# Performance work log

Hardware: AMD Instinct MI355X
Metric: run time of the kernel (lower is better)

The kernel has to match this reference:

```python
import jax, jax.numpy as jnp
import numpy as np
from jax import lax

B, V, M, C, CM, D = 48, 16, 32, 48, 8, 128
VOCAB_V, VOCAB_M, OUT = 2000, 1000, 256


def setup_inputs() -> dict:
    key = jax.random.key(0)
    ks = jax.random.split(key, 22)
    s = 0.1  # keep GRU gates out of saturation
    return {
        "visit_ids": jax.random.randint(ks[0], (3, B, V, C), 0, VOCAB_V),
        "mon_ids": jax.random.randint(ks[1], (4, B, V, M, CM), 0, VOCAB_M),
        "weight_vals": jax.random.uniform(ks[2], (B, V)),
        "age_vals": jax.random.uniform(ks[3], (B, V)),
        "emb_visit": jax.random.normal(ks[4], (3, VOCAB_V, D)) * s,
        "emb_mon": jax.random.normal(ks[5], (4, VOCAB_M, D)) * s,
        "mgru_Wih": jax.random.normal(ks[6], (5, 3 * D, D)) * s,
        "mgru_Whh": jax.random.normal(ks[7], (5, 3 * D, D)) * s,
        "mgru_bih": jax.random.normal(ks[8], (5, 3 * D)) * s,
        "mgru_bhh": jax.random.normal(ks[9], (5, 3 * D)) * s,
        "vgru_Wih": jax.random.normal(ks[10], (7, 3 * D, D)) * s,
        "vgru_Whh": jax.random.normal(ks[11], (7, 3 * D, D)) * s,
        "vgru_bih": jax.random.normal(ks[12], (7, 3 * D)) * s,
        "vgru_bhh": jax.random.normal(ks[13], (7, 3 * D)) * s,
        "fc_weight_w": jax.random.normal(ks[14], (D, 1)) * s,
        "fc_weight_b": jax.random.normal(ks[15], (D,)) * s,
        "fc_age_w": jax.random.normal(ks[16], (D, 1)) * s,
        "fc_age_b": jax.random.normal(ks[17], (D,)) * s,
        "fc_out_w": jax.random.normal(ks[18], (OUT, 7 * D)) * s,
        "fc_out_b": jax.random.normal(ks[19], (OUT,)) * s,
    }


def gru_last(x, Wih, Whh, bih, bhh):
    """torch.nn.GRU(batch_first=True), return final hidden [N, D]."""
    xi = jnp.einsum('ntd,ed->nte', x, Wih) + bih  # [N, T, 3D] input projections
    h0 = jnp.zeros((x.shape[0], Whh.shape[1]), x.dtype)

    def step(h, gi):
        gh = h @ Whh.T + bhh
        ir, iz, inn = jnp.split(gi, 3, axis=-1)
        hr, hz, hn = jnp.split(gh, 3, axis=-1)
        r = jax.nn.sigmoid(ir + hr)
        z = jax.nn.sigmoid(iz + hz)
        n = jnp.tanh(inn + r * hn)
        return (1.0 - z) * n + z * h, None

    hT, _ = lax.scan(step, h0, jnp.swapaxes(xi, 0, 1))
    return hT


def reference(visit_ids, mon_ids, weight_vals, age_vals, emb_visit, emb_mon,
              mgru_Wih, mgru_Whh, mgru_bih, mgru_bhh,
              vgru_Wih, vgru_Whh, vgru_bih, vgru_bhh,
              fc_weight_w, fc_weight_b, fc_age_w, fc_age_b,
              fc_out_w, fc_out_b):
    # padding_idx=0 -> zero embedding row (dropout in eval mode = identity)
    ev = emb_visit.at[:, 0].set(0.0)
    em = emb_mon.at[:, 0].set(0.0)

    # visit-event embedding-bag: sum over code dim -> [B, V, D] per feature
    visit_origin = [jnp.sum(ev[k][visit_ids[k]], axis=2) for k in range(3)]

    def run_stream(t, mi, vi):
        # monitor-level GRU over M, then visit-level GRU over V
        h1 = gru_last(t, mgru_Wih[mi], mgru_Whh[mi], mgru_bih[mi], mgru_bhh[mi])
        h2 = gru_last(h1.reshape(B, V, D),
                      vgru_Wih[vi], vgru_Whh[vi], vgru_bih[vi], vgru_bhh[vi])
        return h2  # [B, D]

    # output slots in dict-insertion order: lab_item, cond, proc, drug, inj_item, weight, age
    slots = [None] * 7
    for p in range(2):  # (lab_item, lab_value), (inj_item, inj_value)
        # elementwise item*value embedding, summed over codes -> [B*V, M, D]
        mon = jnp.sum(em[2 * p][mon_ids[2 * p]] * em[2 * p + 1][mon_ids[2 * p + 1]],
                      axis=3).reshape(B * V, M, D)
        slots[0 if p == 0 else 4] = run_stream(mon, p, p)
        for k in range(3):  # visit features repeated along monitor dim
            t = jnp.broadcast_to(visit_origin[k][:, :, None, :],
                                 (B, V, M, D)).reshape(B * V, M, D)
            h = run_stream(t, 2 + k, 2 + k)
            slots[1 + k] = h if slots[1 + k] is None else slots[1 + k] + h

    # weight / age: Linear(1->D), zero-mask, visit-level GRU
    for vals, w, b, vi, slot in ((weight_vals, fc_weight_w, fc_weight_b, 5, 5),
                                 (age_vals, fc_age_w, fc_age_b, 6, 6)):
        xf = vals.reshape(-1, 1)
        h = (xf @ w.T + b) * (xf != 0)
        slots[slot] = gru_last(h.reshape(B, V, D),
                               vgru_Wih[vi], vgru_Whh[vi], vgru_bih[vi], vgru_bhh[vi])

    patient_emb = jnp.concatenate(slots, axis=-1)  # [B, 7D]
    return jax.nn.relu(patient_emb) @ fc_out_w.T + fc_out_b
```

## Files before the change

### kernel.cpp

```cpp
#include <hip/hip_runtime.h>
#include <stdint.h>


typedef unsigned short u16;
typedef uint32_t u32;
typedef short bf8 __attribute__((ext_vector_type(8)));
typedef float f4 __attribute__((ext_vector_type(4)));

static __device__ __forceinline__ float bf2f(u16 b){ u32 u=((u32)b)<<16; float f; __builtin_memcpy(&f,&u,4); return f; }
static __device__ __forceinline__ u16 f2bf(float f){ u32 u; __builtin_memcpy(&u,&f,4); u32 r=(u+0x7fffu+((u>>16)&1u))>>16; return (u16)r; }
static __device__ __forceinline__ float bflo(u32 u){ u32 x=u<<16; float f; __builtin_memcpy(&f,&x,4); return f; }
static __device__ __forceinline__ float bfhi(u32 u){ u32 x=u&0xffff0000u; float f; __builtin_memcpy(&f,&x,4); return f; }
static __device__ __forceinline__ f4 mfma16(bf8 a, bf8 b, f4 c){ return __builtin_amdgcn_mfma_f32_16x16x32_bf16(a,b,c,0,0,0); }
static __device__ __forceinline__ float sigm(float x){ return 1.0f/(1.0f+__expf(-x)); }
static __device__ __forceinline__ float tanh_f(float x){ return 1.0f-2.0f/(__expf(2.0f*x)+1.0f); }

__global__ __launch_bounds__(256) void k_prep(const float* __restrict__ s0, const float* __restrict__ s1,
                                              const float* __restrict__ s2, const float* __restrict__ s3,
                                              const float* __restrict__ s4,
                                              u16* __restrict__ d0, u16* __restrict__ d1,
                                              u16* __restrict__ d2, u16* __restrict__ d3,
                                              u16* __restrict__ d4){
  int y = blockIdx.y;
  const float* src = y==0?s0 : y==1?s1 : y==2?s2 : y==3?s3 : s4;
  u16* dst         = y==0?d0 : y==1?d1 : y==2?d2 : y==3?d3 : d4;
  int n4 = (y<2 ? 245760 : y<4 ? 344064 : 512000) >> 2;
  int i = blockIdx.x*256 + threadIdx.x;
  if (i < n4){
    float4 v = *(const float4*)(src + (size_t)i*4);
    ushort4 o = { f2bf(v.x), f2bf(v.y), f2bf(v.z), f2bf(v.w) };
    *(ushort4*)(dst + (size_t)i*4) = o;
  }
}

__global__ __launch_bounds__(128) void k_front(const int* __restrict__ vids,
                                               const float* __restrict__ embv,
                                               const float* __restrict__ wv, const float* __restrict__ av,
                                               const float* __restrict__ ww, const float* __restrict__ wb,
                                               const float* __restrict__ aw, const float* __restrict__ ab,
                                               u16* __restrict__ vis_org, u16* __restrict__ hin2T){
  __shared__ int ids[48];
  int y = blockIdx.y, row = blockIdx.x, d = threadIdx.x;
  if (y < 3){
    if (d < 48) ids[d] = vids[((size_t)y*768 + row)*48 + d];
    __syncthreads();
    const float* eb = embv + (size_t)y*2000*128;
    float acc = 0.f;
    #pragma unroll 4
    for (int c = 0; c < 48; ++c){ int id = ids[c]; if (id) acc += eb[(size_t)id*128 + d]; }
    vis_org[((size_t)y*768 + row)*128 + d] = f2bf(acc);
  } else {
    int sidx = y - 3;
    const float* vals = sidx ? av : wv;
    const float* wgt  = sidx ? aw : ww;
    const float* bias = sidx ? ab : wb;
    float v = vals[row];
    float h = (v != 0.f) ? (v * wgt[d] + bias[d]) : 0.f;
    int b = row >> 4, vv = row & 15;
    hin2T[((size_t)(5+sidx)*768 + (size_t)vv*48 + b)*128 + d] = f2bf(h);
  }
}

__global__ __launch_bounds__(256) void k_embed_mon(const int* __restrict__ mids,
                                                   const u16* __restrict__ embm_b,
                                                   u16* __restrict__ mon_xT){
  int p = blockIdx.y;
  int rid = threadIdx.x >> 5, lane32 = threadIdx.x & 31, d0 = lane32*4;
  __shared__ int ids[8][16];
  if (threadIdx.x < 128){
    int rr = threadIdx.x >> 4, c = threadIdx.x & 15;
    int f = 2*p + (c>>3), cm = c & 7;
    ids[rr][c] = mids[((size_t)f*24576 + (size_t)blockIdx.x*8 + rr)*8 + cm];
  }
  __syncthreads();
  const u16* e1 = embm_b + (size_t)(2*p)*1000*128;
  const u16* e2 = embm_b + (size_t)(2*p+1)*1000*128;
  float a0=0.f,a1=0.f,a2=0.f,a3=0.f;
  #pragma unroll
  for (int c = 0; c < 8; ++c){
    int i1 = ids[rid][c], i2 = ids[rid][8+c];
    if (i1 && i2){
      uint2 a = *(const uint2*)(e1 + (size_t)i1*128 + d0);
      uint2 b = *(const uint2*)(e2 + (size_t)i2*128 + d0);
      a0 += bflo(a.x)*bflo(b.x); a1 += bfhi(a.x)*bfhi(b.x);
      a2 += bflo(a.y)*bflo(b.y); a3 += bfhi(a.y)*bfhi(b.y);
    }
  }
  size_t nm = (size_t)blockIdx.x*8 + rid;
  int bv = (int)(nm >> 5), m = (int)(nm & 31);
  ushort4 o = { f2bf(a0), f2bf(a1), f2bf(a2), f2bf(a3) };
  *(ushort4*)(mon_xT + (size_t)p*24576*128 + ((size_t)m*768 + bv)*128 + d0) = o;
}

#define ALOAD(D, tt) { const u16* p_ = ap + (size_t)(tt)*rstride; \
  D[0]=*(const bf8*)(p_); D[1]=*(const bf8*)(p_+32); D[2]=*(const bf8*)(p_+64); D[3]=*(const bf8*)(p_+96); }

#define STEP(D, tt, FIRST) { \
  f4 g0={biv[0],biv[0],biv[0],biv[0]}; \
  f4 g1={biv[1],biv[1],biv[1],biv[1]}; \
  f4 g2={biv[2],biv[2],biv[2],biv[2]}; \
  g0=mfma16(D[0],wfi[0][0],g0); g0=mfma16(D[1],wfi[0][1],g0); \
  g0=mfma16(D[2],wfi[0][2],g0); g0=mfma16(D[3],wfi[0][3],g0); \
  g1=mfma16(D[0],wfi[1][0],g1); g1=mfma16(D[1],wfi[1][1],g1); \
  g1=mfma16(D[2],wfi[1][2],g1); g1=mfma16(D[3],wfi[1][3],g1); \
  g2=mfma16(D[0],wfi[2][0],g2); g2=mfma16(D[1],wfi[2][1],g2); \
  g2=mfma16(D[2],wfi[2][2],g2); g2=mfma16(D[3],wfi[2][3],g2); \
  { int tl_ = ((tt)+2 < T) ? (tt)+2 : 0; ALOAD(D, tl_); } \
  f4 a0={bhv[0],bhv[0],bhv[0],bhv[0]}; \
  f4 a1={bhv[1],bhv[1],bhv[1],bhv[1]}; \
  f4 a2={bhv[2],bhv[2],bhv[2],bhv[2]}; \
  if (!(FIRST)){ \
    bf8 hf0 = *(const bf8*)&hlds[cur][lr][0*32+lq*8]; \
    bf8 hf1 = *(const bf8*)&hlds[cur][lr][1*32+lq*8]; \
    bf8 hf2 = *(const bf8*)&hlds[cur][lr][2*32+lq*8]; \
    bf8 hf3 = *(const bf8*)&hlds[cur][lr][3*32+lq*8]; \
    a0=mfma16(hf0,wfh[0][0],a0); a0=mfma16(hf1,wfh[0][1],a0); \
    a0=mfma16(hf2,wfh[0][2],a0); a0=mfma16(hf3,wfh[0][3],a0); \
    a1=mfma16(hf0,wfh[1][0],a1); a1=mfma16(hf1,wfh[1][1],a1); \
    a1=mfma16(hf2,wfh[1][2],a1); a1=mfma16(hf3,wfh[1][3],a1); \
    a2=mfma16(hf0,wfh[2][0],a2); a2=mfma16(hf1,wfh[2][1],a2); \
    a2=mfma16(hf2,wfh[2][2],a2); a2=mfma16(hf3,wfh[2][3],a2); \
  } \
  int nxt_ = cur ^ 1; \
  _Pragma("unroll") \
  for (int r = 0; r < 4; ++r){ \
    float rr2 = sigm(g0[r] + a0[r]); \
    float zz  = sigm(g1[r] + a1[r]); \
    float nn  = tanh_f(g2[r] + rr2*a2[r]); \
    float hv  = (1.0f - zz)*nn + zz*hp[r]; hp[r] = hv; \
    hlds[nxt_][lq*4+r][w*16+lr] = f2bf(hv); \
  } \
  __syncthreads(); cur = nxt_; }

__global__ __launch_bounds__(512, 1) void k_gru(int mode,
    const u16* __restrict__ Asrc, const u16* __restrict__ Asrc2,
    const u16* __restrict__ Wih, const float* __restrict__ bih,
    const u16* __restrict__ Whh, const float* __restrict__ bhh,
    u16* __restrict__ hout, int T){
  int s = blockIdx.y, g = blockIdx.x;
  const u16* A; size_t rstride; u16* ho; int widx;
  if (mode == 0){
    if (s < 2){ A = Asrc + (size_t)s*24576*128; rstride = 768*128; }
    else      { A = Asrc2 + (size_t)(s-2)*768*128; rstride = 0; }
    widx = s;
    int slot = (0x32140u >> (4*s)) & 15;
    ho = hout + (size_t)slot*768*128;
  } else {
    A = Asrc + (size_t)s*768*128; rstride = 48*128;
    widx = (0x6514320u >> (4*s)) & 15;
    ho = hout + (size_t)s*48*128;
  }
  const u16* Wi = Wih + (size_t)widx*384*128;
  const u16* Wh = Whh + (size_t)widx*384*128;
  const float* bi = bih + (size_t)widx*384;
  const float* bh = bhh + (size_t)widx*384;

  int w = threadIdx.x >> 6, l = threadIdx.x & 63;
  int lr = l & 15, lq = l >> 4;

  bf8 wfi[3][4], wfh[3][4]; float biv[3], bhv[3];
  #pragma unroll
  for (int j = 0; j < 3; ++j){
    int colb = (w + 8*j)*16;
    const u16* wpi = Wi + (size_t)(colb + lr)*128 + lq*8;
    const u16* wph = Wh + (size_t)(colb + lr)*128 + lq*8;
    #pragma unroll
    for (int kt = 0; kt < 4; ++kt){
      wfi[j][kt] = *(const bf8*)(wpi + kt*32);
      wfh[j][kt] = *(const bf8*)(wph + kt*32);
    }
    biv[j] = bi[colb + lr];
    bhv[j] = bh[colb + lr];
  }

  const u16* ap = A + (size_t)(g*16 + lr)*128 + lq*8;
  bf8 AF0[4], AF1[4];
  ALOAD(AF0, 0); ALOAD(AF1, 1);

  __shared__ u16 hlds[2][16][132];
  float hp[4] = {0.f,0.f,0.f,0.f};
  int cur = 0;

  STEP(AF0, 0, true); STEP(AF1, 1, false);
  for (int t = 2; t < T; t += 2){
    STEP(AF0, t, false); STEP(AF1, t+1, false);
  }

  if (mode == 0){
    #pragma unroll
    for (int r = 0; r < 4; ++r)
      ho[((size_t)(lq*4+r)*48 + g)*128 + w*16 + lr] = f2bf(hp[r]);
  } else {
    #pragma unroll
    for (int r = 0; r < 4; ++r)
      ho[((size_t)(g*16 + lq*4 + r))*128 + w*16 + lr] = f2bf(hp[r]);
  }
}

__global__ __launch_bounds__(256) void k_final(const u16* __restrict__ h2,
                                               const float* __restrict__ W,
                                               const float* __restrict__ Bias,
                                               float* __restrict__ out){
  int b = blockIdx.x, t = threadIdx.x;
  __shared__ float emb[896];
  for (int i = t; i < 896; i += 256){
    int j = i >> 7, d = i & 127;
    float v = bf2f(h2[((size_t)j*48 + b)*128 + d]);
    if (j >= 1 && j <= 3) v *= 2.0f;
    emb[i] = fmaxf(v, 0.f);
  }
  __syncthreads();
  float acc = Bias[t];
  const float* wp = W + (size_t)t*896;
  for (int i = 0; i < 896; i += 8){
    float4 w0 = *(const float4*)(wp + i);
    float4 w1 = *(const float4*)(wp + i + 4);
    acc += w0.x*emb[i]   + w0.y*emb[i+1] + w0.z*emb[i+2] + w0.w*emb[i+3];
    acc += w1.x*emb[i+4] + w1.y*emb[i+5] + w1.z*emb[i+6] + w1.w*emb[i+7];
  }
  out[(size_t)b*256 + t] = acc;
}

extern "C" void kernel_launch(void* const* d_in, const int* in_sizes, int n_in,
                              void* d_out, int out_size, void* d_ws, size_t ws_size,
                              hipStream_t stream){
  const int*   visit_ids   = (const int*)d_in[0];
  const int*   mon_ids     = (const int*)d_in[1];
  const float* weight_vals = (const float*)d_in[2];
  const float* age_vals    = (const float*)d_in[3];
  const float* emb_visit   = (const float*)d_in[4];
  const float* emb_mon     = (const float*)d_in[5];
  const float* mgru_Wih    = (const float*)d_in[6];
  const float* mgru_Whh    = (const float*)d_in[7];
  const float* mgru_bih    = (const float*)d_in[8];
  const float* mgru_bhh    = (const float*)d_in[9];
  const float* vgru_Wih    = (const float*)d_in[10];
  const float* vgru_Whh    = (const float*)d_in[11];
  const float* vgru_bih    = (const float*)d_in[12];
  const float* vgru_bhh    = (const float*)d_in[13];
  const float* fc_w_w      = (const float*)d_in[14];
  const float* fc_w_b      = (const float*)d_in[15];
  const float* fc_a_w      = (const float*)d_in[16];
  const float* fc_a_b      = (const float*)d_in[17];
  const float* fc_out_w    = (const float*)d_in[18];
  const float* fc_out_b    = (const float*)d_in[19];

  char* ws = (char*)d_ws;
  size_t o = 0;
  u16* mWih_b  = (u16*)(ws+o); o += 5ull*384*128*2;
  u16* mWhh_b  = (u16*)(ws+o); o += 5ull*384*128*2;
  u16* vWih_b  = (u16*)(ws+o); o += 7ull*384*128*2;
  u16* vWhh_b  = (u16*)(ws+o); o += 7ull*384*128*2;
  u16* embm_b  = (u16*)(ws+o); o += 4ull*1000*128*2;
  u16* mon_xT  = (u16*)(ws+o); o += 2ull*24576*128*2;
  u16* vis_org = (u16*)(ws+o); o += 3ull*768*128*2;
  u16* hin2T   = (u16*)(ws+o); o += 7ull*768*128*2;
  u16* h2      = (u16*)(ws+o); o += 7ull*48*128*2;

  k_prep<<<dim3(500,5), 256, 0, stream>>>(mgru_Wih, mgru_Whh, vgru_Wih, vgru_Whh, emb_mon,
                                          mWih_b, mWhh_b, vWih_b, vWhh_b, embm_b);
  k_front<<<dim3(768,5), 128, 0, stream>>>(visit_ids, emb_visit,
                                           weight_vals, age_vals, fc_w_w, fc_w_b, fc_a_w, fc_a_b,
                                           vis_org, hin2T);
  k_embed_mon<<<dim3(3072,2), 256, 0, stream>>>(mon_ids, embm_b, mon_xT);
  k_gru<<<dim3(48,5), 512, 0, stream>>>(0, mon_xT, vis_org,
                                        mWih_b, mgru_bih, mWhh_b, mgru_bhh, hin2T, 32);
  k_gru<<<dim3(3,7), 512, 0, stream>>>(1, hin2T, (const u16*)0,
                                       vWih_b, vgru_bih, vWhh_b, vgru_bhh, h2, 16);
  k_final<<<48, 256, 0, stream>>>(h2, fc_out_w, fc_out_b, (float*)d_out);
}
```

Baseline: 141.2 us.

## Software-pipeline GRU input projections and hoist constant-input projection out of loop

Restructures the GRU step loop so the input-projection MFMAs for step t+2 are computed after the current gate update, with global loads prefetched four steps ahead. This takes the Wih matmul off the serial recurrence's critical path. When the input is broadcast across time (rstride==0), the input projection is computed once and reused for every step. The barrier now waits only on LDS traffic (lgkmcnt) rather than a full __syncthreads, and launch bounds allow two blocks per CU, which raises register pressure because more accumulator state is held live.

Measured after the change: 146.0 us. 1.03x slower.

```diff
diff --git a/kernel.cpp b/kernel.cpp
--- a/kernel.cpp
+++ b/kernel.cpp
@@ -92,47 +92,63 @@
   *(ushort4*)(mon_xT + (size_t)p*24576*128 + ((size_t)m*768 + bv)*128 + d0) = o;
 }
 
-#define ALOAD(D, tt) { const u16* p_ = ap + (size_t)(tt)*rstride; \
-  D[0]=*(const bf8*)(p_); D[1]=*(const bf8*)(p_+32); D[2]=*(const bf8*)(p_+64); D[3]=*(const bf8*)(p_+96); }
-
-#define STEP(D, tt, FIRST) { \
-  f4 g0={biv[0],biv[0],biv[0],biv[0]}; \
-  f4 g1={biv[1],biv[1],biv[1],biv[1]}; \
-  f4 g2={biv[2],biv[2],biv[2],biv[2]}; \
-  g0=mfma16(D[0],wfi[0][0],g0); g0=mfma16(D[1],wfi[0][1],g0); \
-  g0=mfma16(D[2],wfi[0][2],g0); g0=mfma16(D[3],wfi[0][3],g0); \
-  g1=mfma16(D[0],wfi[1][0],g1); g1=mfma16(D[1],wfi[1][1],g1); \
-  g1=mfma16(D[2],wfi[1][2],g1); g1=mfma16(D[3],wfi[1][3],g1); \
-  g2=mfma16(D[0],wfi[2][0],g2); g2=mfma16(D[1],wfi[2][1],g2); \
-  g2=mfma16(D[2],wfi[2][2],g2); g2=mfma16(D[3],wfi[2][3],g2); \
-  { int tl_ = ((tt)+2 < T) ? (tt)+2 : 0; ALOAD(D, tl_); } \
-  f4 a0={bhv[0],bhv[0],bhv[0],bhv[0]}; \
-  f4 a1={bhv[1],bhv[1],bhv[1],bhv[1]}; \
-  f4 a2={bhv[2],bhv[2],bhv[2],bhv[2]}; \
-  if (!(FIRST)){ \
-    bf8 hf0 = *(const bf8*)&hlds[cur][lr][0*32+lq*8]; \
-    bf8 hf1 = *(const bf8*)&hlds[cur][lr][1*32+lq*8]; \
-    bf8 hf2 = *(const bf8*)&hlds[cur][lr][2*32+lq*8]; \
-    bf8 hf3 = *(const bf8*)&hlds[cur][lr][3*32+lq*8]; \
-    a0=mfma16(hf0,wfh[0][0],a0); a0=mfma16(hf1,wfh[0][1],a0); \
-    a0=mfma16(hf2,wfh[0][2],a0); a0=mfma16(hf3,wfh[0][3],a0); \
-    a1=mfma16(hf0,wfh[1][0],a1); a1=mfma16(hf1,wfh[1][1],a1); \
-    a1=mfma16(hf2,wfh[1][2],a1); a1=mfma16(hf3,wfh[1][3],a1); \
-    a2=mfma16(hf0,wfh[2][0],a2); a2=mfma16(hf1,wfh[2][1],a2); \
-    a2=mfma16(hf2,wfh[2][2],a2); a2=mfma16(hf3,wfh[2][3],a2); \
-  } \
-  int nxt_ = cur ^ 1; \
+
+#define BARRIER() asm volatile("s_waitcnt lgkmcnt(0)\n\ts_barrier" ::: "memory")
+
+#define ALOAD(D, tt) { int t_=(tt); if (t_>=T) t_=0; \
+  const u16* p_ = ap + (size_t)t_*rstride; \
+  D[0]=*(const bf8*)(p_); D[1]=*(const bf8*)(p_+32); \
+  D[2]=*(const bf8*)(p_+64); D[3]=*(const bf8*)(p_+96); }
+
+#define GIMM(G0,G1,G2,D) { \
+  f4 t0_={biv[0],biv[0],biv[0],biv[0]}; G0=t0_; \
+  f4 t1_={biv[1],biv[1],biv[1],biv[1]}; G1=t1_; \
+  f4 t2_={biv[2],biv[2],biv[2],biv[2]}; G2=t2_; \
+  G0=mfma16(D[0],wfi[0][0],G0); G0=mfma16(D[1],wfi[0][1],G0); \
+  G0=mfma16(D[2],wfi[0][2],G0); G0=mfma16(D[3],wfi[0][3],G0); \
+  G1=mfma16(D[0],wfi[1][0],G1); G1=mfma16(D[1],wfi[1][1],G1); \
+  G1=mfma16(D[2],wfi[1][2],G1); G1=mfma16(D[3],wfi[1][3],G1); \
+  G2=mfma16(D[0],wfi[2][0],G2); G2=mfma16(D[1],wfi[2][1],G2); \
+  G2=mfma16(D[2],wfi[2][2],G2); G2=mfma16(D[3],wfi[2][3],G2); }
+
+#define GHRD() \
+  bf8 hf0_=*(const bf8*)&hlds[cur][lr][lq*8]; \
+  bf8 hf1_=*(const bf8*)&hlds[cur][lr][32+lq*8]; \
+  bf8 hf2_=*(const bf8*)&hlds[cur][lr][64+lq*8]; \
+  bf8 hf3_=*(const bf8*)&hlds[cur][lr][96+lq*8]; \
+  f4 a0_={bhv[0],bhv[0],bhv[0],bhv[0]}; \
+  f4 a1_={bhv[1],bhv[1],bhv[1],bhv[1]}; \
+  f4 a2_={bhv[2],bhv[2],bhv[2],bhv[2]}; \
+  a0_=mfma16(hf0_,wfh[0][0],a0_); a0_=mfma16(hf1_,wfh[0][1],a0_); \
+  a0_=mfma16(hf2_,wfh[0][2],a0_); a0_=mfma16(hf3_,wfh[0][3],a0_); \
+  a1_=mfma16(hf0_,wfh[1][0],a1_); a1_=mfma16(hf1_,wfh[1][1],a1_); \
+  a1_=mfma16(hf2_,wfh[1][2],a1_); a1_=mfma16(hf3_,wfh[1][3],a1_); \
+  a2_=mfma16(hf0_,wfh[2][0],a2_); a2_=mfma16(hf1_,wfh[2][1],a2_); \
+  a2_=mfma16(hf2_,wfh[2][2],a2_); a2_=mfma16(hf3_,wfh[2][3],a2_);
+
+#define GATES(G0,G1,G2) { int nxt_=cur^1; \
   _Pragma("unroll") \
-  for (int r = 0; r < 4; ++r){ \
-    float rr2 = sigm(g0[r] + a0[r]); \
-    float zz  = sigm(g1[r] + a1[r]); \
-    float nn  = tanh_f(g2[r] + rr2*a2[r]); \
-    float hv  = (1.0f - zz)*nn + zz*hp[r]; hp[r] = hv; \
-    hlds[nxt_][lq*4+r][w*16+lr] = f2bf(hv); \
-  } \
-  __syncthreads(); cur = nxt_; }
-
-__global__ __launch_bounds__(512, 1) void k_gru(int mode,
+  for (int r=0;r<4;++r){ \
+    float rr_=sigm(G0[r]+a0_[r]); \
+    float zz_=sigm(G1[r]+a1_[r]); \
+    float nn_=tanh_f(G2[r]+rr_*a2_[r]); \
+    float hv_=(1.0f-zz_)*nn_+zz_*hp[r]; hp[r]=hv_; \
+    hlds[nxt_][lq*4+r][w*16+lr]=f2bf(hv_); } \
+  BARRIER(); cur=nxt_; }
+
+#define STEP0(G0,G1,G2) { \
+  f4 a0_={bhv[0],bhv[0],bhv[0],bhv[0]}; \
+  f4 a1_={bhv[1],bhv[1],bhv[1],bhv[1]}; \
+  f4 a2_={bhv[2],bhv[2],bhv[2],bhv[2]}; \
+  GATES(G0,G1,G2); }
+
+#define STEPB(G0,G1,G2,SN,tt) { \
+  GHRD(); \
+  GATES(G0,G1,G2); \
+  if ((tt)+2 < T){ GIMM(G0,G1,G2,SN); } \
+  ALOAD(SN,(tt)+4); }
+
+__global__ __launch_bounds__(512, 2) void k_gru(int mode,
     const u16* __restrict__ Asrc, const u16* __restrict__ Asrc2,
     const u16* __restrict__ Wih, const float* __restrict__ bih,
     const u16* __restrict__ Whh, const float* __restrict__ bhh,
@@ -174,16 +190,33 @@
   }
 
   const u16* ap = A + (size_t)(g*16 + lr)*128 + lq*8;
-  bf8 AF0[4], AF1[4];
-  ALOAD(AF0, 0); ALOAD(AF1, 1);
-
   __shared__ u16 hlds[2][16][132];
   float hp[4] = {0.f,0.f,0.f,0.f};
   int cur = 0;
 
-  STEP(AF0, 0, true); STEP(AF1, 1, false);
-  for (int t = 2; t < T; t += 2){
-    STEP(AF0, t, false); STEP(AF1, t+1, false);
+  if (rstride){
+    bf8 S0[4], S1[4];
+    f4 gE0,gE1,gE2, gO0,gO1,gO2;
+    ALOAD(S0,0); ALOAD(S1,1);
+    GIMM(gE0,gE1,gE2,S0); ALOAD(S0,2);
+    GIMM(gO0,gO1,gO2,S1); ALOAD(S1,3);
+    STEP0(gE0,gE1,gE2);
+    GIMM(gE0,gE1,gE2,S0); ALOAD(S0,4);
+    STEPB(gO0,gO1,gO2,S1,1);
+    for (int t = 2; t < T; t += 2){
+      STEPB(gE0,gE1,gE2,S0,t);
+      STEPB(gO0,gO1,gO2,S1,t+1);
+    }
+  } else {
+    bf8 S0[4];
+    f4 gE0,gE1,gE2;
+    ALOAD(S0,0);
+    GIMM(gE0,gE1,gE2,S0);
+    STEP0(gE0,gE1,gE2);
+    for (int t = 1; t < T; ++t){
+      GHRD();
+      GATES(gE0,gE1,gE2);
+    }
   }
 
   if (mode == 0){
```
